# Kernel tuning notes

Hardware: AMD Instinct MI355X
Metric: run time of the kernel (lower is better)

Reference implementation:

```python
import jax, jax.numpy as jnp
import numpy as np
from jax import lax

EPS = 1e-6

def _ln2d(x, w, b):
    # LayerNorm over channel dim (axis=1), per pixel
    mu = jnp.mean(x, axis=1, keepdims=True)
    var = jnp.mean((x - mu) ** 2, axis=1, keepdims=True)
    xn = (x - mu) / jnp.sqrt(var + EPS)
    return xn * w[None, :, None, None] + b[None, :, None, None]

def _sg(x):
    x1, x2 = jnp.split(x, 2, axis=1)
    return x1 * x2

def _conv1x1_per_sample(x, w, b):
    # x: [B,C,H,W], w: [B,O,C,1,1], b: [B,O]
    y = jnp.einsum('bchw,boc->bohw', x, w[..., 0, 0])
    return y + b[:, :, None, None]

def _dwconv3x3_per_sample(x, w, b):
    # x: [B,C,H,W], w: [B,C,1,3,3] -> grouped conv with B*C groups
    B, C, H, W = x.shape
    xr = x.reshape(1, B * C, H, W)
    k = w.reshape(B * C, 1, 3, 3)
    y = lax.conv_general_dilated(xr, k, (1, 1), ((1, 1), (1, 1)),
                                 feature_group_count=B * C,
                                 dimension_numbers=('NCHW', 'OIHW', 'NCHW'))
    return y.reshape(B, C, H, W) + b[:, :, None, None]

def setup_inputs() -> dict:
    key = jax.random.key(0)
    ks = jax.random.split(key, 12)
    B, c, H, W = 16, 32, 256, 256
    dw, ffn = 2 * c, 2 * c
    s = 0.05
    return {
        'inp': jax.random.normal(ks[0], (B, c, H, W), jnp.float32),
        'w1': jax.random.normal(ks[1], (B, dw, c, 1, 1), jnp.float32) * s,
        'b1': jax.random.normal(ks[2], (B, dw), jnp.float32) * s,
        'w2': jax.random.normal(ks[3], (B, dw, 1, 3, 3), jnp.float32) * s,
        'b2': jax.random.normal(ks[4], (B, dw), jnp.float32) * s,
        'w3': jax.random.normal(ks[5], (B, c, dw // 2, 1, 1), jnp.float32) * s,
        'b3': jax.random.normal(ks[6], (B, c), jnp.float32) * s,
        'w4': jax.random.normal(ks[7], (B, ffn, c, 1, 1), jnp.float32) * s,
        'b4': jax.random.normal(ks[8], (B, ffn), jnp.float32) * s,
        'w5': jax.random.normal(ks[9], (B, c, ffn // 2, 1, 1), jnp.float32) * s,
        'b5': jax.random.normal(ks[10], (B, c), jnp.float32) * s,
        'n1_w': jnp.ones((c,), jnp.float32),
        'n1_b': jnp.zeros((c,), jnp.float32),
        'n2_w': jnp.ones((c,), jnp.float32),
        'n2_b': jnp.zeros((c,), jnp.float32),
        'sca_w': jax.random.normal(ks[11], (dw // 2, dw // 2, 1, 1), jnp.float32) * s,
        'sca_b': jnp.zeros((dw // 2,), jnp.float32),
        'beta': jnp.zeros((1, c, 1, 1), jnp.float32),
        'gamma': jnp.zeros((1, c, 1, 1), jnp.float32),
    }

def reference(inp, w1, b1, w2, b2, w3, b3, w4, b4, w5, b5,
              n1_w, n1_b, n2_w, n2_b, sca_w, sca_b, beta, gamma):
    x = _ln2d(inp, n1_w, n1_b)
    x = _conv1x1_per_sample(x, w1, b1)          # [B, dw, H, W]
    x = _dwconv3x3_per_sample(x, w2, b2)        # [B, dw, H, W]
    x = _sg(x)                                  # [B, dw/2, H, W]
    # SE / simplified channel attention
    s = jnp.mean(x, axis=(2, 3))                # [B, dw/2]
    s = jnp.einsum('bc,oc->bo', s, sca_w[..., 0, 0]) + sca_b
    x = x * s[:, :, None, None]
    x = _conv1x1_per_sample(x, w3, b3)          # [B, c, H, W]
    y = inp + x * beta
    x = _ln2d(y, n2_w, n2_b)
    x = _conv1x1_per_sample(x, w4, b4)          # [B, ffn, H, W]
    x = _sg(x)                                  # [B, ffn/2, H, W]
    x = _conv1x1_per_sample(x, w5, b5)          # [B, c, H, W]
    return y + x * gamma
```

## Files before the change

kernel.cpp:

```cpp
#include <hip/hip_runtime.h>

typedef unsigned short u16;
typedef unsigned int   u32;
typedef __attribute__((ext_vector_type(8))) short short8;
typedef __attribute__((ext_vector_type(4))) float f32x4;

#define DI static __device__ __forceinline__


static constexpr int OFF_SSUM = 0;
static constexpr int OFF_SCALE = 512;
static constexpr int OFF_W1 = 1024;
static constexpr int OFF_B1 = 33792;
static constexpr int OFF_W2 = 34816;
static constexpr int OFF_B2 = 44032;
static constexpr int OFF_W3 = 45056;
static constexpr int OFF_B3 = 61440;
static constexpr int OFF_W4 = 61952;
static constexpr int OFF_B4 = 94720;
static constexpr int OFF_W5 = 95744;
static constexpr int OFF_B5 = 112128;
static constexpr int OFF_N1W = 112640;
static constexpr int OFF_N1B = 112672;
static constexpr int OFF_N2W = 112704;
static constexpr int OFF_N2B = 112736;
static constexpr int OFF_SCAW = 112768;
static constexpr int OFF_SCAB = 113792;
static constexpr int OFF_BETA = 113824;
static constexpr int OFF_GAMMA = 113856;
static constexpr int OFF_PART = 113920;

DI u16 f2bf(float f) {
  u32 x = __float_as_uint(f);
  u32 r = (x + 0x7fffu + ((x >> 16) & 1u)) >> 16;
  return (u16)r;
}

struct WPtrs {
  const float *w1, *b1, *w2, *b2, *w3, *b3, *w4, *b4, *w5, *b5;
  const float *n1w, *n1b, *n2w, *n2b, *scaw, *scab, *beta, *gamma;
};

DI void cpy_seg(float* dst, const float* src, int n, int tid, int stride) {
  for (int i = tid; i < n; i += stride) dst[i] = src[i];
}

__global__ __launch_bounds__(256) void k_pack(WPtrs p, float* __restrict__ wf) {
  const int tid = blockIdx.x * 256 + threadIdx.x;
  const int stride = gridDim.x * 256;
  cpy_seg(wf + OFF_W1, p.w1, 32768, tid, stride);
  cpy_seg(wf + OFF_B1, p.b1, 1024, tid, stride);
  cpy_seg(wf + OFF_W2, p.w2, 9216, tid, stride);
  cpy_seg(wf + OFF_B2, p.b2, 1024, tid, stride);
  cpy_seg(wf + OFF_W3, p.w3, 16384, tid, stride);
  cpy_seg(wf + OFF_B3, p.b3, 512, tid, stride);
  cpy_seg(wf + OFF_W4, p.w4, 32768, tid, stride);
  cpy_seg(wf + OFF_B4, p.b4, 1024, tid, stride);
  cpy_seg(wf + OFF_W5, p.w5, 16384, tid, stride);
  cpy_seg(wf + OFF_B5, p.b5, 512, tid, stride);
  cpy_seg(wf + OFF_N1W, p.n1w, 32, tid, stride);
  cpy_seg(wf + OFF_N1B, p.n1b, 32, tid, stride);
  cpy_seg(wf + OFF_N2W, p.n2w, 32, tid, stride);
  cpy_seg(wf + OFF_N2B, p.n2b, 32, tid, stride);
  cpy_seg(wf + OFF_SCAW, p.scaw, 1024, tid, stride);
  cpy_seg(wf + OFF_SCAB, p.scab, 32, tid, stride);
  cpy_seg(wf + OFF_BETA, p.beta, 32, tid, stride);
  cpy_seg(wf + OFF_GAMMA, p.gamma, 32, tid, stride);
}

__global__ __launch_bounds__(256) void k_front(const float* __restrict__ inp,
                                               const float* __restrict__ wf,
                                               float* __restrict__ x3,
                                               float* __restrict__ part) {
  const int tid = threadIdx.x;
  const int b = blockIdx.y;
  const int tile = blockIdx.x;
  const int tx = tile & 7, ty = tile >> 3;
  const int gx0 = tx * 32 - 1, gy0 = ty * 8 - 1;

  __shared__ u16 xln[352][40];
  __shared__ u32 x1p[32][340];
  __shared__ float psum[4][32];

  const float* w1 = wf + OFF_W1 + b * 2048;
  const float* b1 = wf + OFF_B1 + b * 64;
  const float* n1w = wf + OFF_N1W;
  const float* n1b = wf + OFF_N1B;

#pragma unroll 1
  for (int idx = tid; idx < 352; idx += 256) {
    const int py = idx / 34;
    const int px = idx - py * 34;
    const int gy = gy0 + py, gx = gx0 + px;
    u32 pk[16];
    if (idx >= 340 || (u32)gy >= 256u || (u32)gx >= 256u) {
#pragma unroll
      for (int j = 0; j < 16; j++) pk[j] = 0u;
    } else {
      const float* src = inp + (((size_t)(b * 32)) << 16) + (gy << 8) + gx;
      float x[32];
      float s = 0.f, s2 = 0.f;
#pragma unroll
      for (int c = 0; c < 32; c++) {
        float v = src[(size_t)c << 16];
        x[c] = v; s += v; s2 += v * v;
      }
      const float mu = s * (1.f / 32.f);
      const float var = fmaxf(s2 * (1.f / 32.f) - mu * mu, 0.f);
      const float rstd = rsqrtf(var + 1e-6f);
#pragma unroll
      for (int j = 0; j < 16; j++) {
        const float lo = (x[2 * j] - mu) * rstd * n1w[2 * j] + n1b[2 * j];
        const float hi = (x[2 * j + 1] - mu) * rstd * n1w[2 * j + 1] + n1b[2 * j + 1];
        pk[j] = (u32)f2bf(lo) | ((u32)f2bf(hi) << 16);
      }
    }
    u32* row = (u32*)&xln[idx][0];
#pragma unroll
    for (int q = 0; q < 4; q++)
      *(uint4*)(row + 4 * q) = make_uint4(pk[4 * q], pk[4 * q + 1], pk[4 * q + 2], pk[4 * q + 3]);
  }

  const int lane = tid & 63;
  const int wv = tid >> 6;
  const int lr = lane & 15;
  const int lq = lane >> 4;

  short8 w1f[4];
#pragma unroll
  for (int t = 0; t < 4; t++) {
    const float* wp = w1 + (t * 16 + lr) * 32 + 8 * lq;
    short8 f;
#pragma unroll
    for (int j = 0; j < 8; j++) f[j] = (short)f2bf(wp[j]);
    w1f[t] = f;
  }
  float b1v[4];
#pragma unroll
  for (int t = 0; t < 4; t++) b1v[t] = b1[t * 16 + lr];

  __syncthreads();

  const f32x4 zero = {0.f, 0.f, 0.f, 0.f};
#pragma unroll 1
  for (int g = wv; g < 22; g += 4) {
    const short8 af = *(const short8*)&xln[16 * g + lr][8 * lq];
    f32x4 d0 = __builtin_amdgcn_mfma_f32_16x16x32_bf16(af, w1f[0], zero, 0, 0, 0);
    f32x4 d1 = __builtin_amdgcn_mfma_f32_16x16x32_bf16(af, w1f[1], zero, 0, 0, 0);
    f32x4 d2 = __builtin_amdgcn_mfma_f32_16x16x32_bf16(af, w1f[2], zero, 0, 0, 0);
    f32x4 d3 = __builtin_amdgcn_mfma_f32_16x16x32_bf16(af, w1f[3], zero, 0, 0, 0);
#pragma unroll
    for (int r = 0; r < 4; r++) {
      const int pix = 16 * g + 4 * lq + r;
      if (pix < 340) {
        const int py = pix / 34;
        const int px = pix - 34 * py;
        const int gy = gy0 + py, gx = gx0 + px;
        u32 v0 = 0u, v1 = 0u;
        if (((u32)gy < 256u) & ((u32)gx < 256u)) {
          v0 = (u32)f2bf(d0[r] + b1v[0]) | ((u32)f2bf(d2[r] + b1v[2]) << 16);
          v1 = (u32)f2bf(d1[r] + b1v[1]) | ((u32)f2bf(d3[r] + b1v[3]) << 16);
        }
        x1p[lr][pix] = v0;
        x1p[lr + 16][pix] = v1;
      }
    }
  }
  __syncthreads();

  const int px = tid & 31, py = tid >> 5;
  const int p = (py + 1) * 34 + (px + 1);
  const int gpix = ((ty * 8 + py) << 8) + (tx * 32 + px);
  const float* w2 = wf + OFF_W2 + b * 576;
  const float* b2 = wf + OFF_B2 + b * 64;
  float* ob = x3 + (((size_t)(b * 32)) << 16) + gpix;

#pragma unroll 2
  for (int c = 0; c < 32; c++) {
    float a1 = b2[c], a2 = b2[c + 32];
    const int offs[9] = {-35, -34, -33, -1, 0, 1, 33, 34, 35};
#pragma unroll
    for (int k = 0; k < 9; k++) {
      const u32 u = x1p[c][p + offs[k]];
      const float lo = __uint_as_float(u << 16);
      const float hi = __uint_as_float(u & 0xffff0000u);
      a1 += lo * w2[c * 9 + k];
      a2 += hi * w2[(c + 32) * 9 + k];
    }
    const float v = a1 * a2;
    ob[(size_t)c << 16] = v;
    float r = v;
#pragma unroll
    for (int off = 32; off > 0; off >>= 1) r += __shfl_xor(r, off, 64);
    if ((tid & 63) == 0) psum[wv][c] = r;
  }
  __syncthreads();

  if (tid < 32) {
    const float t4 = psum[0][tid] + psum[1][tid] + psum[2][tid] + psum[3][tid];
    part[(((b << 8) + tile) << 5) + tid] = t4;
  }
}

__global__ __launch_bounds__(256) void k_sca(float* __restrict__ wf) {
  const int b = blockIdx.x;
  const int tid = threadIdx.x;
  const int q = tid >> 5, c = tid & 31;
  __shared__ float l[8][32];
  __shared__ float sv[32];
  const float* part = wf + OFF_PART + b * 8192;
  float a = 0.f;
#pragma unroll 4
  for (int t = q; t < 256; t += 8) a += part[t * 32 + c];
  l[q][c] = a;
  __syncthreads();
  if (tid < 32) {
    float s = 0.f;
#pragma unroll
    for (int qq = 0; qq < 8; qq++) s += l[qq][tid];
    sv[tid] = s * (1.f / 65536.f);
  }
  __syncthreads();
  if (tid < 32) {
    const float* sw = wf + OFF_SCAW;
    float acc = wf[OFF_SCAB + tid];
#pragma unroll
    for (int cc = 0; cc < 32; cc++) acc += sv[cc] * sw[tid * 32 + cc];
    wf[OFF_SCALE + b * 32 + tid] = acc;
  }
}

__global__ __launch_bounds__(256) void k_back(const float* __restrict__ inp,
                                              const float* x3,
                                              const float* __restrict__ wf,
                                              float* out) {
  const int tid = threadIdx.x;
  const int b = blockIdx.y;
  const int wv = tid >> 6;
  const int lane = tid & 63;
  const int lr = lane & 15;
  const int lq = lane >> 4;

  __shared__ u16 tbuf[4][16][40];

  const size_t ib = ((size_t)(b * 32)) << 16;
  const float* w3 = wf + OFF_W3 + b * 1024;
  const float* w4 = wf + OFF_W4 + b * 2048;
  const float* w5 = wf + OFF_W5 + b * 1024;

  short8 w3f[2], w4f[4], w5f[2];
#pragma unroll
  for (int t = 0; t < 2; t++) {
    const float* wp = w3 + (t * 16 + lr) * 32 + 8 * lq;
    short8 f;
#pragma unroll
    for (int j = 0; j < 8; j++) f[j] = (short)f2bf(wp[j]);
    w3f[t] = f;
  }
#pragma unroll
  for (int t = 0; t < 4; t++) {
    const float* wp = w4 + (t * 16 + lr) * 32 + 8 * lq;
    short8 f;
#pragma unroll
    for (int j = 0; j < 8; j++) f[j] = (short)f2bf(wp[j]);
    w4f[t] = f;
  }
#pragma unroll
  for (int t = 0; t < 2; t++) {
    const float* wp = w5 + (t * 16 + lr) * 32 + 8 * lq;
    short8 f;
#pragma unroll
    for (int j = 0; j < 8; j++) f[j] = (short)f2bf(wp[j]);
    w5f[t] = f;
  }

  float scv[8];
#pragma unroll
  for (int j = 0; j < 8; j++) scv[j] = wf[OFF_SCALE + b * 32 + 8 * lq + j];

  float b3v[2], bev[2], n2wv[2], n2bv[2], b5v[2], gav[2], b4v[4];
#pragma unroll
  for (int t = 0; t < 2; t++) {
    b3v[t]  = wf[OFF_B3 + b * 32 + lr + 16 * t];
    bev[t]  = wf[OFF_BETA + lr + 16 * t];
    n2wv[t] = wf[OFF_N2W + lr + 16 * t];
    n2bv[t] = wf[OFF_N2B + lr + 16 * t];
    b5v[t]  = wf[OFF_B5 + b * 32 + lr + 16 * t];
    gav[t]  = wf[OFF_GAMMA + lr + 16 * t];
  }
#pragma unroll
  for (int t = 0; t < 4; t++) b4v[t] = wf[OFF_B4 + b * 64 + lr + 16 * t];

  const f32x4 zero = {0.f, 0.f, 0.f, 0.f};

#pragma unroll 1
  for (int it = 0; it < 4; it++) {
    const int P0 = blockIdx.x * 256 + wv * 64 + it * 16;

    short8 xaf;
#pragma unroll
    for (int j = 0; j < 8; j++) {
      float v = x3[ib + (((size_t)(8 * lq + j)) << 16) + P0 + lr] * scv[j];
      xaf[j] = (short)f2bf(v);
    }

    f32x4 d0 = __builtin_amdgcn_mfma_f32_16x16x32_bf16(xaf, w3f[0], zero, 0, 0, 0);
    f32x4 d1 = __builtin_amdgcn_mfma_f32_16x16x32_bf16(xaf, w3f[1], zero, 0, 0, 0);

    float y[2][4], s[4], s2[4];
#pragma unroll
    for (int t = 0; t < 2; t++) {
      const f32x4 iv = *(const f32x4*)(inp + ib + (((size_t)(lr + 16 * t)) << 16) + P0 + 4 * lq);
      const f32x4 dd = t ? d1 : d0;
#pragma unroll
      for (int r = 0; r < 4; r++) y[t][r] = iv[r] + (dd[r] + b3v[t]) * bev[t];
    }
#pragma unroll
    for (int r = 0; r < 4; r++) {
      s[r]  = y[0][r] + y[1][r];
      s2[r] = y[0][r] * y[0][r] + y[1][r] * y[1][r];
    }
#pragma unroll
    for (int m = 1; m <= 8; m <<= 1) {
#pragma unroll
      for (int r = 0; r < 4; r++) {
        s[r]  += __shfl_xor(s[r], m, 64);
        s2[r] += __shfl_xor(s2[r], m, 64);
      }
    }
    float mu[4], rstd[4];
#pragma unroll
    for (int r = 0; r < 4; r++) {
      mu[r] = s[r] * (1.f / 32.f);
      const float var = fmaxf(s2[r] * (1.f / 32.f) - mu[r] * mu[r], 0.f);
      rstd[r] = rsqrtf(var + 1e-6f);
    }

#pragma unroll
    for (int t = 0; t < 2; t++) {
#pragma unroll
      for (int r = 0; r < 4; r++) {
        const float zz = (y[t][r] - mu[r]) * rstd[r] * n2wv[t] + n2bv[t];
        tbuf[wv][4 * lq + r][lr + 16 * t] = f2bf(zz);
      }
    }
    const short8 zf = *(const short8*)&tbuf[wv][lr][8 * lq];

    f32x4 e0 = __builtin_amdgcn_mfma_f32_16x16x32_bf16(zf, w4f[0], zero, 0, 0, 0);
    f32x4 e1 = __builtin_amdgcn_mfma_f32_16x16x32_bf16(zf, w4f[1], zero, 0, 0, 0);
    f32x4 e2 = __builtin_amdgcn_mfma_f32_16x16x32_bf16(zf, w4f[2], zero, 0, 0, 0);
    f32x4 e3 = __builtin_amdgcn_mfma_f32_16x16x32_bf16(zf, w4f[3], zero, 0, 0, 0);

#pragma unroll
    for (int t = 0; t < 2; t++) {
      const f32x4 ea = t ? e1 : e0;
      const f32x4 eb = t ? e3 : e2;
#pragma unroll
      for (int r = 0; r < 4; r++) {
        const float gg = (ea[r] + b4v[t]) * (eb[r] + b4v[t + 2]);
        tbuf[wv][4 * lq + r][lr + 16 * t] = f2bf(gg);
      }
    }
    const short8 gf = *(const short8*)&tbuf[wv][lr][8 * lq];

    f32x4 f0 = __builtin_amdgcn_mfma_f32_16x16x32_bf16(gf, w5f[0], zero, 0, 0, 0);
    f32x4 f1 = __builtin_amdgcn_mfma_f32_16x16x32_bf16(gf, w5f[1], zero, 0, 0, 0);

#pragma unroll
    for (int t = 0; t < 2; t++) {
      const f32x4 ff = t ? f1 : f0;
      f32x4 ov;
#pragma unroll
      for (int r = 0; r < 4; r++) ov[r] = y[t][r] + (ff[r] + b5v[t]) * gav[t];
      *(f32x4*)(out + ib + (((size_t)(lr + 16 * t)) << 16) + P0 + 4 * lq) = ov;
    }
  }
}

extern "C" void kernel_launch(void* const* d_in, const int* in_sizes, int n_in,
                              void* d_out, int out_size, void* d_ws, size_t ws_size,
                              hipStream_t stream) {
  (void)in_sizes; (void)n_in; (void)out_size; (void)ws_size;
  const float* inp = (const float*)d_in[0];
  WPtrs p;
  p.w1 = (const float*)d_in[1];  p.b1 = (const float*)d_in[2];
  p.w2 = (const float*)d_in[3];  p.b2 = (const float*)d_in[4];
  p.w3 = (const float*)d_in[5];  p.b3 = (const float*)d_in[6];
  p.w4 = (const float*)d_in[7];  p.b4 = (const float*)d_in[8];
  p.w5 = (const float*)d_in[9];  p.b5 = (const float*)d_in[10];
  p.n1w = (const float*)d_in[11]; p.n1b = (const float*)d_in[12];
  p.n2w = (const float*)d_in[13]; p.n2b = (const float*)d_in[14];
  p.scaw = (const float*)d_in[15]; p.scab = (const float*)d_in[16];
  p.beta = (const float*)d_in[17]; p.gamma = (const float*)d_in[18];

  float* wf = (float*)d_ws;
  float* x3 = (float*)d_out;
  float* out = (float*)d_out;

  k_pack<<<dim3(128), dim3(256), 0, stream>>>(p, wf);
  k_front<<<dim3(256, 16), dim3(256), 0, stream>>>(inp, wf, x3, wf + OFF_PART);
  k_sca<<<dim3(16), dim3(256), 0, stream>>>(wf);
  k_back<<<dim3(256, 16), dim3(256), 0, stream>>>(inp, x3, wf, out);
}
```

Before: 536.7 us.

## Split front kernel into two channel phases to halve conv1x1 LDS buffer

The front kernel now computes the 1x1 conv output in two phases of 16 packed channel pairs each, followed each time by the depthwise 3x3 and gate for those channels. The intermediate LDS buffer shrinks from 32 to 16 rows, with the row stride padded to 341 to avoid bank conflicts. The smaller shared memory footprint is meant to allow more resident blocks per CU. It costs extra barriers and a serialized MFMA/stencil alternation, and the dwconv loop unroll goes from 2 to 4.

```diff
diff --git a/kernel.cpp b/kernel.cpp
--- a/kernel.cpp
+++ b/kernel.cpp
@@ -79,7 +79,7 @@
   const int gx0 = tx * 32 - 1, gy0 = ty * 8 - 1;
 
   __shared__ u16 xln[352][40];
-  __shared__ u32 x1p[32][340];
+  __shared__ u32 x1h[16][341];
   __shared__ float psum[4][32];
 
   const float* w1 = wf + OFF_W1 + b * 2048;
@@ -139,62 +139,62 @@
 #pragma unroll
   for (int t = 0; t < 4; t++) b1v[t] = b1[t * 16 + lr];
 
-  __syncthreads();
-
-  const f32x4 zero = {0.f, 0.f, 0.f, 0.f};
-#pragma unroll 1
-  for (int g = wv; g < 22; g += 4) {
-    const short8 af = *(const short8*)&xln[16 * g + lr][8 * lq];
-    f32x4 d0 = __builtin_amdgcn_mfma_f32_16x16x32_bf16(af, w1f[0], zero, 0, 0, 0);
-    f32x4 d1 = __builtin_amdgcn_mfma_f32_16x16x32_bf16(af, w1f[1], zero, 0, 0, 0);
-    f32x4 d2 = __builtin_amdgcn_mfma_f32_16x16x32_bf16(af, w1f[2], zero, 0, 0, 0);
-    f32x4 d3 = __builtin_amdgcn_mfma_f32_16x16x32_bf16(af, w1f[3], zero, 0, 0, 0);
-#pragma unroll
-    for (int r = 0; r < 4; r++) {
-      const int pix = 16 * g + 4 * lq + r;
-      if (pix < 340) {
-        const int py = pix / 34;
-        const int px = pix - 34 * py;
-        const int gy = gy0 + py, gx = gx0 + px;
-        u32 v0 = 0u, v1 = 0u;
-        if (((u32)gy < 256u) & ((u32)gx < 256u)) {
-          v0 = (u32)f2bf(d0[r] + b1v[0]) | ((u32)f2bf(d2[r] + b1v[2]) << 16);
-          v1 = (u32)f2bf(d1[r] + b1v[1]) | ((u32)f2bf(d3[r] + b1v[3]) << 16);
-        }
-        x1p[lr][pix] = v0;
-        x1p[lr + 16][pix] = v1;
-      }
-    }
-  }
-  __syncthreads();
-
-  const int px = tid & 31, py = tid >> 5;
-  const int p = (py + 1) * 34 + (px + 1);
-  const int gpix = ((ty * 8 + py) << 8) + (tx * 32 + px);
+  const int cpx = tid & 31, cpy = tid >> 5;
+  const int p = (cpy + 1) * 34 + (cpx + 1);
+  const int gpix = ((ty * 8 + cpy) << 8) + (tx * 32 + cpx);
   const float* w2 = wf + OFF_W2 + b * 576;
   const float* b2 = wf + OFF_B2 + b * 64;
   float* ob = x3 + (((size_t)(b * 32)) << 16) + gpix;
 
-#pragma unroll 2
-  for (int c = 0; c < 32; c++) {
-    float a1 = b2[c], a2 = b2[c + 32];
-    const int offs[9] = {-35, -34, -33, -1, 0, 1, 33, 34, 35};
-#pragma unroll
-    for (int k = 0; k < 9; k++) {
-      const u32 u = x1p[c][p + offs[k]];
-      const float lo = __uint_as_float(u << 16);
-      const float hi = __uint_as_float(u & 0xffff0000u);
-      a1 += lo * w2[c * 9 + k];
-      a2 += hi * w2[(c + 32) * 9 + k];
-    }
-    const float v = a1 * a2;
-    ob[(size_t)c << 16] = v;
-    float r = v;
-#pragma unroll
-    for (int off = 32; off > 0; off >>= 1) r += __shfl_xor(r, off, 64);
-    if ((tid & 63) == 0) psum[wv][c] = r;
-  }
   __syncthreads();
+
+  const f32x4 zero = {0.f, 0.f, 0.f, 0.f};
+
+#pragma unroll 1
+  for (int ph = 0; ph < 2; ph++) {
+#pragma unroll 1
+    for (int g = wv; g < 22; g += 4) {
+      const short8 af = *(const short8*)&xln[16 * g + lr][8 * lq];
+      f32x4 dA = __builtin_amdgcn_mfma_f32_16x16x32_bf16(af, w1f[ph], zero, 0, 0, 0);
+      f32x4 dB = __builtin_amdgcn_mfma_f32_16x16x32_bf16(af, w1f[ph + 2], zero, 0, 0, 0);
+#pragma unroll
+      for (int r = 0; r < 4; r++) {
+        const int pix = 16 * g + 4 * lq + r;
+        if (pix < 340) {
+          const int py = pix / 34;
+          const int px = pix - 34 * py;
+          const int gy = gy0 + py, gx = gx0 + px;
+          u32 v = 0u;
+          if (((u32)gy < 256u) & ((u32)gx < 256u))
+            v = (u32)f2bf(dA[r] + b1v[ph]) | ((u32)f2bf(dB[r] + b1v[ph + 2]) << 16);
+          x1h[lr][pix] = v;
+        }
+      }
+    }
+    __syncthreads();
+
+#pragma unroll 4
+    for (int cc = 0; cc < 16; cc++) {
+      const int c = ph * 16 + cc;
+      float a1 = b2[c], a2 = b2[c + 32];
+      const int offs[9] = {-35, -34, -33, -1, 0, 1, 33, 34, 35};
+#pragma unroll
+      for (int k = 0; k < 9; k++) {
+        const u32 u = x1h[cc][p + offs[k]];
+        const float lo = __uint_as_float(u << 16);
+        const float hi = __uint_as_float(u & 0xffff0000u);
+        a1 += lo * w2[c * 9 + k];
+        a2 += hi * w2[(c + 32) * 9 + k];
+      }
+      const float v = a1 * a2;
+      ob[(size_t)c << 16] = v;
+      float r = v;
+#pragma unroll
+      for (int off = 32; off > 0; off >>= 1) r += __shfl_xor(r, off, 64);
+      if ((tid & 63) == 0) psum[wv][c] = r;
+    }
+    __syncthreads();
+  }
 
   if (tid < 32) {
     const float t4 = psum[0][tid] + psum[1][tid] + psum[2][tid] + psum[3][tid];
```

After: 514.4 us. 1.04x faster.
